# Performance work log

Hardware: AMD Instinct MI355X
Metric: run time of the kernel (lower is better)

Reference implementation:

```python
import jax, jax.numpy as jnp
import numpy as np

S, B, D, H, F = 2048, 4, 1024, 2, 2048
HD = D // H  # head dim = 512
EPS = 1e-8   # forward() hardcodes 1e-8, ignoring init eps


def rmsnorm(x, w):
    ms = jnp.mean(x * x, axis=-1, keepdims=True)
    return w * (x / jnp.sqrt(ms + EPS))


def setup_inputs() -> dict:
    key = jax.random.key(0)
    ks = jax.random.split(key, 12)
    s = 0.02
    return {
        "x": jax.random.normal(ks[0], (S, B, D), jnp.float32),
        "w_norm1": 1.0 + s * jax.random.normal(ks[1], (D,), jnp.float32),
        "in_proj_w": s * jax.random.normal(ks[2], (3 * D, D), jnp.float32),
        "in_proj_b": s * jax.random.normal(ks[3], (3 * D,), jnp.float32),
        "out_proj_w": s * jax.random.normal(ks[4], (D, D), jnp.float32),
        "out_proj_b": s * jax.random.normal(ks[5], (D,), jnp.float32),
        "w_norm2": 1.0 + s * jax.random.normal(ks[6], (D,), jnp.float32),
        "W1": s * jax.random.normal(ks[7], (F, D), jnp.float32),
        "b1": s * jax.random.normal(ks[8], (F,), jnp.float32),
        "W2": s * jax.random.normal(ks[9], (D, F), jnp.float32),
        "b2": s * jax.random.normal(ks[10], (D,), jnp.float32),
    }


def reference(x, w_norm1, in_proj_w, in_proj_b, out_proj_w, out_proj_b,
              w_norm2, W1, b1, W2, b2):
    # pre-norm
    h = rmsnorm(x, w_norm1)                      # (S,B,D)
    # packed qkv projection (torch MultiheadAttention in_proj)
    qkv = h @ in_proj_w.T + in_proj_b            # (S,B,3D)
    q, k, v = jnp.split(qkv, 3, axis=-1)
    # (S,B,D) -> (B,H,S,HD)
    def heads(t):
        return t.reshape(S, B, H, HD).transpose(1, 2, 0, 3)
    q, k, v = heads(q), heads(k), heads(v)
    scores = jnp.einsum("bhsd,bhtd->bhst", q, k) / jnp.sqrt(jnp.float32(HD))
    causal = jnp.tril(jnp.ones((S, S), bool))
    scores = jnp.where(causal, scores, -jnp.inf)
    attn = jax.nn.softmax(scores, axis=-1)       # (B,H,S,S)
    ctx = jnp.einsum("bhst,bhtd->bhsd", attn, v)  # (B,H,S,HD)
    ctx = ctx.transpose(2, 0, 1, 3).reshape(S, B, D)
    attn_out = ctx @ out_proj_w.T + out_proj_b
    # residual 1
    x1 = x + attn_out
    # MLP: Linear -> exact GELU -> Linear
    m = rmsnorm(x1, w_norm2)
    mlp = jax.nn.gelu(m @ W1.T + b1, approximate=False) @ W2.T + b2
    return x1 + mlp
```

## Files before the change

kernel.cpp:

```cpp
#include <hip/hip_runtime.h>


typedef __bf16 bf16;
typedef bf16 bf16x8 __attribute__((ext_vector_type(8)));
typedef bf16 bf16x4 __attribute__((ext_vector_type(4)));
typedef float f32x4 __attribute__((ext_vector_type(4)));

#define MFMA16x16x32(A, B, C) __builtin_amdgcn_mfma_f32_16x16x32_bf16(A, B, C, 0, 0, 0)

__device__ __forceinline__ void gload16(const void* g, void* l) {
  __builtin_amdgcn_global_load_lds(
      (const __attribute__((address_space(1))) void*)g,
      (__attribute__((address_space(3))) void*)l, 16, 0, 0);
}

__global__ __launch_bounds__(256) void wcvt(
    const float* __restrict__ src, bf16* __restrict__ dst, int n)
{
  const int i = (blockIdx.x * 256 + threadIdx.x) * 4;
  if (i < n) {
    const float4 v = *(const float4*)(src + i);
    bf16x4 o;
    o[0] = (bf16)v.x; o[1] = (bf16)v.y; o[2] = (bf16)v.z; o[3] = (bf16)v.w;
    *(bf16x4*)(dst + i) = o;
  }
}

__global__ __launch_bounds__(256) void rmsnorm_kernel(
    const float* __restrict__ x, const float* __restrict__ w, bf16* __restrict__ out)
{
  const int row = blockIdx.x;
  const int tid = threadIdx.x;
  const float4 v = *(const float4*)(x + (size_t)row * 1024 + tid * 4);
  float ss = v.x * v.x + v.y * v.y + v.z * v.z + v.w * v.w;
#pragma unroll
  for (int off = 1; off < 64; off <<= 1) ss += __shfl_xor(ss, off, 64);
  __shared__ float red[4];
  if ((tid & 63) == 0) red[tid >> 6] = ss;
  __syncthreads();
  const float tot = red[0] + red[1] + red[2] + red[3];
  const float inv = rsqrtf(tot * (1.0f / 1024.0f) + 1e-8f);
  const float4 g = *(const float4*)(w + tid * 4);
  bf16x4 o;
  o[0] = (bf16)(v.x * g.x * inv);
  o[1] = (bf16)(v.y * g.y * inv);
  o[2] = (bf16)(v.z * g.z * inv);
  o[3] = (bf16)(v.w * g.w * inv);
  *(bf16x4*)(out + (size_t)row * 1024 + tid * 4) = o;
}

enum { EPI_BF16 = 0, EPI_RES = 1, EPI_GELU = 2, EPI_QKV = 3 };

template <int EPI>
__global__ __launch_bounds__(256, 3) void gemm_bt2(
    const bf16* __restrict__ A,
    const bf16* __restrict__ B,
    const float* __restrict__ bias,
    const float* res,
    float* outF, bf16* outQ, bf16* outK, bf16* outV,
    int M, int N, int K)
{
  __shared__ bf16 As[128 * 32];
  __shared__ bf16 Bs[128 * 32];
  const int tid = threadIdx.x;
  const int Nb = N >> 7;
  const int lin = blockIdx.x;
  const int sup = lin / (Nb << 4);
  const int rem = lin - sup * (Nb << 4);
  const int bm = (sup << 4) + (rem & 15);
  const int bn = rem >> 4;
  const int w = tid >> 6, lane = tid & 63;
  const int q = lane >> 4, lr = lane & 15;
  const int wr = (w >> 1) * 64, wc = (w & 1) * 64;
  f32x4 acc[4][4] = {};
  const int srow = lane >> 2;
  const int gch = ((lane & 3) - ((lane >> 3) & 3)) & 3;
  const bf16* Ab = A + (size_t)(bm * 128) * K;
  const bf16* Bb = B + (size_t)(bn * 128) * K;
  const int sw = ((q + (lr >> 1)) & 3) * 16;

  for (int k0 = 0; k0 < K; k0 += 32) {
    __syncthreads();
#pragma unroll
    for (int c = 0; c < 2; c++) {
      const int r = (w * 2 + c) * 16 + srow;
      gload16(Ab + (size_t)r * K + k0 + gch * 8, &As[(w * 2 + c) * 512]);
      gload16(Bb + (size_t)r * K + k0 + gch * 8, &Bs[(w * 2 + c) * 512]);
    }
    __syncthreads();
    bf16x8 af[4], bfr[4];
#pragma unroll
    for (int mt = 0; mt < 4; mt++)
      af[mt] = *(const bf16x8*)((const char*)As + (wr + mt * 16 + lr) * 64 + sw);
#pragma unroll
    for (int nt = 0; nt < 4; nt++)
      bfr[nt] = *(const bf16x8*)((const char*)Bs + (wc + nt * 16 + lr) * 64 + sw);
#pragma unroll
    for (int mt = 0; mt < 4; mt++)
#pragma unroll
      for (int nt = 0; nt < 4; nt++)
        acc[mt][nt] = MFMA16x16x32(af[mt], bfr[nt], acc[mt][nt]);
  }
  const int gm0 = bm * 128 + wr + q * 4;
  const int gn0 = bn * 128 + wc + lr;
  bf16* outs = nullptr;
  if constexpr (EPI == EPI_QKV) {
    const int reg = (bn * 128) >> 10;
    outs = reg == 0 ? outQ : (reg == 1 ? outK : outV);
  } else {
    outs = outQ;
  }
#pragma unroll
  for (int nt = 0; nt < 4; nt++) {
    const int gn = gn0 + nt * 16;
    const float bv = bias[gn];
#pragma unroll
    for (int mt = 0; mt < 4; mt++) {
#pragma unroll
      for (int r = 0; r < 4; r++) {
        float v = acc[mt][nt][r] + bv;
        const int gm = gm0 + mt * 16 + r;
        if constexpr (EPI == EPI_GELU) {
          v = 0.5f * v * (1.0f + erff(v * 0.70710678118654752f));
          outs[(size_t)gm * N + gn] = (bf16)v;
        } else if constexpr (EPI == EPI_BF16) {
          outs[(size_t)gm * N + gn] = (bf16)v;
        } else if constexpr (EPI == EPI_QKV) {
          outs[(size_t)gm * 1024 + (gn & 1023)] = (bf16)v;
        } else {
          const size_t idx = (size_t)gm * N + gn;
          outF[idx] = v + res[idx];
        }
      }
    }
  }
}

__global__ __launch_bounds__(256) void vtrans_kernel(
    const bf16* __restrict__ vtmp, bf16* __restrict__ vt)
{
  __shared__ bf16 tile[64 * 72];
  const int kt = blockIdx.x;
  const int dt = blockIdx.y;
  const int bh = blockIdx.z;
  const int b = bh >> 1, h = bh & 1;
  const int tid = threadIdx.x;
#pragma unroll
  for (int it = 0; it < 2; it++) {
    const int key = it * 32 + (tid >> 3);
    const int dc = (tid & 7) * 8;
    const bf16x8 v = *(const bf16x8*)(vtmp +
        (size_t)((kt * 64 + key) * 4 + b) * 1024 + h * 512 + dt * 64 + dc);
    *(bf16x8*)&tile[key * 72 + dc] = v;
  }
  __syncthreads();
#pragma unroll
  for (int it = 0; it < 2; it++) {
    const int dim = it * 32 + (tid >> 3);
    const int kc = (tid & 7) * 8;
    bf16x8 o;
#pragma unroll
    for (int j = 0; j < 8; j++) o[j] = tile[(kc + j) * 72 + dim];
    *(bf16x8*)(vt + (size_t)bh * (1u << 20) +
               (size_t)(dt * 64 + dim) * 2048 + kt * 64 + kc) = o;
  }
}

__global__ __launch_bounds__(512, 2) void attn_kernel(
    const bf16* __restrict__ qb, const bf16* __restrict__ kb,
    const bf16* __restrict__ vtg, bf16* __restrict__ opart,
    float* __restrict__ lpart)
{
  __shared__ bf16 Ks[2][32 * 520];
  __shared__ bf16 Ps[2][4][16 * 40];
  const int bh = blockIdx.x;
  const int i = blockIdx.y;
  const int half = i >= 32;
  const int qt = half ? 63 - i : i;
  const int b = bh >> 1, h = bh & 1;
  const int tid = threadIdx.x;
  const int w = tid >> 6, lane = tid & 63;
  const int q = lane >> 4, lr = lane & 15;
  const int qrow0 = qt * 64;
  const int c0 = half ? (qt + 1) : 0;
  const int c1 = c0 + (qt + 1);
  const float sc = 0.044194173824159216f;

  if (w < 4) {
    bf16x8 Qf[16];
    {
      const bf16* qp = qb + (size_t)((qrow0 + w * 16 + lr) * 4 + b) * 1024 + h * 512 + q * 8;
#pragma unroll
      for (int kk = 0; kk < 16; kk++) Qf[kk] = *(const bf16x8*)(qp + kk * 32);
    }
    const bf16* krow0 = kb + (size_t)b * 1024 + h * 512 + lane * 8;
#pragma unroll
    for (int j = 0; j < 8; j++)
      gload16(krow0 + (size_t)((c0 * 32 + w * 8 + j) * 4) * 1024,
              &Ks[c0 & 1][(w * 8 + j) * 520]);
    __syncthreads();
    const int myrow = qrow0 + w * 16 + q * 4;
    for (int t = c0; t <= c1; t++) {
      if (t < c1) {
        const int p = t & 1;
        const int kc = t * 32;
        if (t + 1 < c1) {
          const int kc2 = (t + 1) * 32;
#pragma unroll
          for (int j = 0; j < 8; j++)
            gload16(krow0 + (size_t)((kc2 + w * 8 + j) * 4) * 1024,
                    &Ks[1 - p][(w * 8 + j) * 520]);
        }
        const bool dead = kc > qrow0 + w * 16 + 15;
        float p0[4], p1[4];
        if (!dead) {
          f32x4 S0 = {}, S1 = {};
#pragma unroll
          for (int kk = 0; kk < 16; kk++) {
            const bf16x8 k0 = *(const bf16x8*)&Ks[p][lr * 520 + kk * 32 + q * 8];
            const bf16x8 k1 = *(const bf16x8*)&Ks[p][(16 + lr) * 520 + kk * 32 + q * 8];
            S0 = MFMA16x16x32(Qf[kk], k0, S0);
            S1 = MFMA16x16x32(Qf[kk], k1, S1);
          }
#pragma unroll
          for (int r = 0; r < 4; r++) {
            const int row = myrow + r;
            p0[r] = (kc + lr > row) ? 0.f : __expf(S0[r] * sc);
            p1[r] = (kc + 16 + lr > row) ? 0.f : __expf(S1[r] * sc);
          }
        } else {
#pragma unroll
          for (int r = 0; r < 4; r++) { p0[r] = 0.f; p1[r] = 0.f; }
        }
#pragma unroll
        for (int r = 0; r < 4; r++) {
          Ps[p][w][(q * 4 + r) * 40 + lr] = (bf16)p0[r];
          Ps[p][w][(q * 4 + r) * 40 + 16 + lr] = (bf16)p1[r];
        }
      }
      __syncthreads();
    }
  } else {
    const int pw = w - 4;
    f32x4 O[4][8] = {};
    f32x4 lac = {};
    bf16x8 ones;
#pragma unroll
    for (int e = 0; e < 8; e++) ones[e] = (bf16)1.0f;
    const bf16* vbase = vtg + ((size_t)bh << 20) + (size_t)(pw * 128 + lr) * 2048 + q * 8;
    __syncthreads();
    for (int t = c0; t <= c1; t++) {
      if (t > c0) {
        const int p = (t - 1) & 1;
        const int kc = (t - 1) * 32;
        bf16x8 pa[4];
#pragma unroll
        for (int rt = 0; rt < 4; rt++)
          pa[rt] = *(const bf16x8*)&Ps[p][rt][lr * 40 + q * 8];
        lac = MFMA16x16x32(pa[pw], ones, lac);
#pragma unroll
        for (int ct = 0; ct < 8; ct++) {
          const bf16x8 vf = *(const bf16x8*)(vbase + (size_t)(ct * 16) * 2048 + kc);
#pragma unroll
          for (int rt = 0; rt < 4; rt++)
            O[rt][ct] = MFMA16x16x32(pa[rt], vf, O[rt][ct]);
        }
      }
      __syncthreads();
    }
    bf16* op = opart + (size_t)half * (8u << 20) + (size_t)bh * (1u << 20);
#pragma unroll
    for (int rt = 0; rt < 4; rt++)
#pragma unroll
      for (int ct = 0; ct < 8; ct++)
#pragma unroll
        for (int r = 0; r < 4; r++)
          op[(size_t)(qrow0 + rt * 16 + q * 4 + r) * 512 + pw * 128 + ct * 16 + lr] =
              (bf16)O[rt][ct][r];
    if (lr == 0) {
#pragma unroll
      for (int r = 0; r < 4; r++)
        lpart[half * 16384 + bh * 2048 + qrow0 + pw * 16 + q * 4 + r] = lac[r];
    }
  }
}

__global__ __launch_bounds__(256) void attn_combine(
    const bf16* __restrict__ opart, const float* __restrict__ lpart,
    bf16* __restrict__ ctx)
{
  const int gid = blockIdx.x * 256 + threadIdx.x;
  const int bh = gid >> 17;
  const int rem = gid & 131071;
  const int row = rem >> 6;
  const int dc = (rem & 63) * 8;
  const size_t o = (size_t)bh * (1u << 20) + (size_t)row * 512 + dc;
  const bf16x8 a = *(const bf16x8*)(opart + o);
  const bf16x8 c = *(const bf16x8*)(opart + (size_t)(8u << 20) + o);
  const float inv = 1.0f /
      (lpart[bh * 2048 + row] + lpart[16384 + bh * 2048 + row]);
  bf16x8 ov;
#pragma unroll
  for (int e = 0; e < 8; e++) ov[e] = (bf16)(((float)a[e] + (float)c[e]) * inv);
  const int b = bh >> 1, h = bh & 1;
  *(bf16x8*)(ctx + (size_t)(row * 4 + b) * 1024 + h * 512 + dc) = ov;
}

extern "C" void kernel_launch(void* const* d_in, const int* in_sizes, int n_in,
                              void* d_out, int out_size, void* d_ws, size_t ws_size,
                              hipStream_t stream)
{
  (void)in_sizes; (void)n_in; (void)out_size; (void)ws_size;
  const float* x    = (const float*)d_in[0];
  const float* wn1  = (const float*)d_in[1];
  const float* wqkv = (const float*)d_in[2];
  const float* bqkv = (const float*)d_in[3];
  const float* wout = (const float*)d_in[4];
  const float* bout = (const float*)d_in[5];
  const float* wn2  = (const float*)d_in[6];
  const float* W1   = (const float*)d_in[7];
  const float* b1   = (const float*)d_in[8];
  const float* W2   = (const float*)d_in[9];
  const float* b2   = (const float*)d_in[10];
  float* out = (float*)d_out;

  char* ws = (char*)d_ws;
  const size_t Mi = 1u << 20;
  bf16* S0v = (bf16*)(ws);
  bf16* S1v = (bf16*)(ws + 16 * Mi);
  bf16* S2v = (bf16*)(ws + 32 * Mi);
  bf16* S3v = (bf16*)(ws + 48 * Mi);
  bf16* wqb = (bf16*)(ws + 64 * Mi);
  bf16* wob = (bf16*)(ws + 70 * Mi);
  bf16* w1b = (bf16*)(ws + 72 * Mi);
  bf16* w2b = (bf16*)(ws + 76 * Mi);
  const int M = 8192;

  wcvt<<<3072, 256, 0, stream>>>(wqkv, wqb, 3145728);
  wcvt<<<1024, 256, 0, stream>>>(wout, wob, 1048576);
  wcvt<<<2048, 256, 0, stream>>>(W1, w1b, 2097152);
  wcvt<<<2048, 256, 0, stream>>>(W2, w2b, 2097152);
  rmsnorm_kernel<<<8192, 256, 0, stream>>>(x, wn1, S0v);
  gemm_bt2<EPI_QKV><<<64 * 24, 256, 0, stream>>>(
      S0v, wqb, bqkv, nullptr, nullptr, S1v, S2v, S3v, M, 3072, 1024);
  vtrans_kernel<<<dim3(32, 8, 8), 256, 0, stream>>>(S3v, S0v);
  attn_kernel<<<dim3(8, 64), 512, 0, stream>>>(
      S1v, S2v, S0v, (bf16*)d_out, (float*)S3v);
  attn_combine<<<4096, 256, 0, stream>>>((const bf16*)d_out, (const float*)S3v, S1v);
  gemm_bt2<EPI_RES><<<64 * 8, 256, 0, stream>>>(
      S1v, wob, bout, x, out, nullptr, nullptr, nullptr, M, 1024, 1024);
  rmsnorm_kernel<<<8192, 256, 0, stream>>>(out, wn2, S0v);
  gemm_bt2<EPI_GELU><<<64 * 16, 256, 0, stream>>>(
      S0v, w1b, b1, nullptr, nullptr, S2v, nullptr, nullptr, M, 2048, 1024);
  gemm_bt2<EPI_RES><<<64 * 8, 256, 0, stream>>>(
      S2v, w2b, b2, out, out, nullptr, nullptr, nullptr, M, 1024, 2048);
}
```

Measured before the change: 480.0 us.

## Process two attention work items per block and double-buffer V fragments in registers

The attention kernel now runs both work halves (query tile j and 31-j) serially inside one block, halving the grid to 256 blocks and relaxing launch bounds to one block per CU. The PV warps now prefetch the next V tile into a register double buffer before the MFMA loop, so global V loads overlap with the current tile's matrix multiplies. This trades occupancy for more registers, which allows the prefetch, and evens out causal work per block. Fewer resident blocks may hide latency less well.

```diff
diff --git a/kernel.cpp b/kernel.cpp
--- a/kernel.cpp
+++ b/kernel.cpp
@@ -166,7 +166,7 @@
   }
 }
 
-__global__ __launch_bounds__(512, 2) void attn_kernel(
+__global__ __launch_bounds__(512, 1) void attn_kernel(
     const bf16* __restrict__ qb, const bf16* __restrict__ kb,
     const bf16* __restrict__ vtg, bf16* __restrict__ opart,
     float* __restrict__ lpart)
@@ -174,113 +174,124 @@
   __shared__ bf16 Ks[2][32 * 520];
   __shared__ bf16 Ps[2][4][16 * 40];
   const int bh = blockIdx.x;
-  const int i = blockIdx.y;
-  const int half = i >= 32;
-  const int qt = half ? 63 - i : i;
+  const int j = blockIdx.y;
   const int b = bh >> 1, h = bh & 1;
   const int tid = threadIdx.x;
   const int w = tid >> 6, lane = tid & 63;
   const int q = lane >> 4, lr = lane & 15;
-  const int qrow0 = qt * 64;
-  const int c0 = half ? (qt + 1) : 0;
-  const int c1 = c0 + (qt + 1);
   const float sc = 0.044194173824159216f;
 
-  if (w < 4) {
-    bf16x8 Qf[16];
-    {
-      const bf16* qp = qb + (size_t)((qrow0 + w * 16 + lr) * 4 + b) * 1024 + h * 512 + q * 8;
-#pragma unroll
-      for (int kk = 0; kk < 16; kk++) Qf[kk] = *(const bf16x8*)(qp + kk * 32);
-    }
-    const bf16* krow0 = kb + (size_t)b * 1024 + h * 512 + lane * 8;
-#pragma unroll
-    for (int j = 0; j < 8; j++)
-      gload16(krow0 + (size_t)((c0 * 32 + w * 8 + j) * 4) * 1024,
-              &Ks[c0 & 1][(w * 8 + j) * 520]);
-    __syncthreads();
-    const int myrow = qrow0 + w * 16 + q * 4;
-    for (int t = c0; t <= c1; t++) {
-      if (t < c1) {
-        const int p = t & 1;
-        const int kc = t * 32;
-        if (t + 1 < c1) {
-          const int kc2 = (t + 1) * 32;
-#pragma unroll
-          for (int j = 0; j < 8; j++)
-            gload16(krow0 + (size_t)((kc2 + w * 8 + j) * 4) * 1024,
-                    &Ks[1 - p][(w * 8 + j) * 520]);
+  for (int item = 0; item < 2; item++) {
+    const int half = item;
+    const int qt = item ? (31 - j) : j;
+    const int qrow0 = qt * 64;
+    const int c0 = item ? (qt + 1) : 0;
+    const int c1 = c0 + (qt + 1);
+
+    if (w < 4) {
+      bf16x8 Qf[16];
+      {
+        const bf16* qp = qb + (size_t)((qrow0 + w * 16 + lr) * 4 + b) * 1024 + h * 512 + q * 8;
+#pragma unroll
+        for (int kk = 0; kk < 16; kk++) Qf[kk] = *(const bf16x8*)(qp + kk * 32);
+      }
+      const bf16* krow0 = kb + (size_t)b * 1024 + h * 512 + lane * 8;
+#pragma unroll
+      for (int jj = 0; jj < 8; jj++)
+        gload16(krow0 + (size_t)((c0 * 32 + w * 8 + jj) * 4) * 1024,
+                &Ks[c0 & 1][(w * 8 + jj) * 520]);
+      __syncthreads();
+      const int myrow = qrow0 + w * 16 + q * 4;
+      for (int t = c0; t <= c1; t++) {
+        if (t < c1) {
+          const int p = t & 1;
+          const int kc = t * 32;
+          if (t + 1 < c1) {
+            const int kc2 = (t + 1) * 32;
+#pragma unroll
+            for (int jj = 0; jj < 8; jj++)
+              gload16(krow0 + (size_t)((kc2 + w * 8 + jj) * 4) * 1024,
+                      &Ks[1 - p][(w * 8 + jj) * 520]);
+          }
+          const bool deadc = kc > qrow0 + w * 16 + 15;
+          float p0[4], p1[4];
+          if (!deadc) {
+            f32x4 S0 = {}, S1 = {};
+#pragma unroll
+            for (int kk = 0; kk < 16; kk++) {
+              const bf16x8 k0 = *(const bf16x8*)&Ks[p][lr * 520 + kk * 32 + q * 8];
+              const bf16x8 k1 = *(const bf16x8*)&Ks[p][(16 + lr) * 520 + kk * 32 + q * 8];
+              S0 = MFMA16x16x32(Qf[kk], k0, S0);
+              S1 = MFMA16x16x32(Qf[kk], k1, S1);
+            }
+#pragma unroll
+            for (int r = 0; r < 4; r++) {
+              const int row = myrow + r;
+              p0[r] = (kc + lr > row) ? 0.f : __expf(S0[r] * sc);
+              p1[r] = (kc + 16 + lr > row) ? 0.f : __expf(S1[r] * sc);
+            }
+          } else {
+#pragma unroll
+            for (int r = 0; r < 4; r++) { p0[r] = 0.f; p1[r] = 0.f; }
+          }
+#pragma unroll
+          for (int r = 0; r < 4; r++) {
+            Ps[p][w][(q * 4 + r) * 40 + lr] = (bf16)p0[r];
+            Ps[p][w][(q * 4 + r) * 40 + 16 + lr] = (bf16)p1[r];
+          }
         }
-        const bool dead = kc > qrow0 + w * 16 + 15;
-        float p0[4], p1[4];
-        if (!dead) {
-          f32x4 S0 = {}, S1 = {};
-#pragma unroll
-          for (int kk = 0; kk < 16; kk++) {
-            const bf16x8 k0 = *(const bf16x8*)&Ks[p][lr * 520 + kk * 32 + q * 8];
-            const bf16x8 k1 = *(const bf16x8*)&Ks[p][(16 + lr) * 520 + kk * 32 + q * 8];
-            S0 = MFMA16x16x32(Qf[kk], k0, S0);
-            S1 = MFMA16x16x32(Qf[kk], k1, S1);
-          }
-#pragma unroll
-          for (int r = 0; r < 4; r++) {
-            const int row = myrow + r;
-            p0[r] = (kc + lr > row) ? 0.f : __expf(S0[r] * sc);
-            p1[r] = (kc + 16 + lr > row) ? 0.f : __expf(S1[r] * sc);
-          }
-        } else {
-#pragma unroll
-          for (int r = 0; r < 4; r++) { p0[r] = 0.f; p1[r] = 0.f; }
+        __syncthreads();
+      }
+    } else {
+      const int pw = w - 4;
+      f32x4 O[4][8] = {};
+      f32x4 lac = {};
+      bf16x8 ones;
+#pragma unroll
+      for (int e = 0; e < 8; e++) ones[e] = (bf16)1.0f;
+      const bf16* vbase = vtg + ((size_t)bh << 20) + (size_t)(pw * 128 + lr) * 2048 + q * 8;
+      bf16x8 vf[2][8];
+#pragma unroll
+      for (int ct = 0; ct < 8; ct++)
+        vf[0][ct] = *(const bf16x8*)(vbase + (size_t)(ct * 16) * 2048 + c0 * 32);
+      __syncthreads();
+      for (int t = c0; t <= c1; t++) {
+        if (t > c0 && t < c1) {
+          const int nb = (t - c0) & 1;
+#pragma unroll
+          for (int ct = 0; ct < 8; ct++)
+            vf[nb][ct] = *(const bf16x8*)(vbase + (size_t)(ct * 16) * 2048 + t * 32);
         }
-#pragma unroll
-        for (int r = 0; r < 4; r++) {
-          Ps[p][w][(q * 4 + r) * 40 + lr] = (bf16)p0[r];
-          Ps[p][w][(q * 4 + r) * 40 + 16 + lr] = (bf16)p1[r];
+        if (t > c0) {
+          const int p = (t - 1) & 1;
+          const int cb = (t - 1 - c0) & 1;
+          bf16x8 pa[4];
+#pragma unroll
+          for (int rt = 0; rt < 4; rt++)
+            pa[rt] = *(const bf16x8*)&Ps[p][rt][lr * 40 + q * 8];
+          lac = MFMA16x16x32(pa[pw], ones, lac);
+#pragma unroll
+          for (int ct = 0; ct < 8; ct++)
+#pragma unroll
+            for (int rt = 0; rt < 4; rt++)
+              O[rt][ct] = MFMA16x16x32(pa[rt], vf[cb][ct], O[rt][ct]);
         }
-      }
-      __syncthreads();
-    }
-  } else {
-    const int pw = w - 4;
-    f32x4 O[4][8] = {};
-    f32x4 lac = {};
-    bf16x8 ones;
-#pragma unroll
-    for (int e = 0; e < 8; e++) ones[e] = (bf16)1.0f;
-    const bf16* vbase = vtg + ((size_t)bh << 20) + (size_t)(pw * 128 + lr) * 2048 + q * 8;
-    __syncthreads();
-    for (int t = c0; t <= c1; t++) {
-      if (t > c0) {
-        const int p = (t - 1) & 1;
-        const int kc = (t - 1) * 32;
-        bf16x8 pa[4];
-#pragma unroll
-        for (int rt = 0; rt < 4; rt++)
-          pa[rt] = *(const bf16x8*)&Ps[p][rt][lr * 40 + q * 8];
-        lac = MFMA16x16x32(pa[pw], ones, lac);
-#pragma unroll
-        for (int ct = 0; ct < 8; ct++) {
-          const bf16x8 vf = *(const bf16x8*)(vbase + (size_t)(ct * 16) * 2048 + kc);
-#pragma unroll
-          for (int rt = 0; rt < 4; rt++)
-            O[rt][ct] = MFMA16x16x32(pa[rt], vf, O[rt][ct]);
-        }
-      }
-      __syncthreads();
-    }
-    bf16* op = opart + (size_t)half * (8u << 20) + (size_t)bh * (1u << 20);
-#pragma unroll
-    for (int rt = 0; rt < 4; rt++)
-#pragma unroll
-      for (int ct = 0; ct < 8; ct++)
+        __syncthreads();
+      }
+      bf16* op = opart + (size_t)half * (8u << 20) + (size_t)bh * (1u << 20);
+#pragma unroll
+      for (int rt = 0; rt < 4; rt++)
+#pragma unroll
+        for (int ct = 0; ct < 8; ct++)
+#pragma unroll
+          for (int r = 0; r < 4; r++)
+            op[(size_t)(qrow0 + rt * 16 + q * 4 + r) * 512 + pw * 128 + ct * 16 + lr] =
+                (bf16)O[rt][ct][r];
+      if (lr == 0) {
 #pragma unroll
         for (int r = 0; r < 4; r++)
-          op[(size_t)(qrow0 + rt * 16 + q * 4 + r) * 512 + pw * 128 + ct * 16 + lr] =
-              (bf16)O[rt][ct][r];
-    if (lr == 0) {
-#pragma unroll
-      for (int r = 0; r < 4; r++)
-        lpart[half * 16384 + bh * 2048 + qrow0 + pw * 16 + q * 4 + r] = lac[r];
+          lpart[half * 16384 + bh * 2048 + qrow0 + pw * 16 + q * 4 + r] = lac[r];
+      }
     }
   }
 }
@@ -344,7 +355,7 @@
   gemm_bt2<EPI_QKV><<<64 * 24, 256, 0, stream>>>(
       S0v, wqb, bqkv, nullptr, nullptr, S1v, S2v, S3v, M, 3072, 1024);
   vtrans_kernel<<<dim3(32, 8, 8), 256, 0, stream>>>(S3v, S0v);
-  attn_kernel<<<dim3(8, 64), 512, 0, stream>>>(
+  attn_kernel<<<dim3(8, 32), 512, 0, stream>>>(
       S1v, S2v, S0v, (bf16*)d_out, (float*)S3v);
   attn_combine<<<4096, 256, 0, stream>>>((const bf16*)d_out, (const float*)S3v, S1v);
   gemm_bt2<EPI_RES><<<64 * 8, 256, 0, stream>>>(
```

New measurement: 534.2 us. +11.3%, slower.
